# Kernel tuning notes

Measured on AMD Instinct MI355X. Metric: run time of the kernel, lower is better.

The kernel has to match this reference:

```python
import jax, jax.numpy as jnp
import numpy as np

DIM = 1024
NUM_HEADS = 16
NUM_KV_HEADS = 4
HEAD_DIM = DIM // NUM_HEADS  # 64
QK_GAIN = 1.5
ROPE_BASE = 10000.0


def _rms_norm(x, eps):
    # F.rms_norm with no weight: x / sqrt(mean(x^2) + eps)
    ms = jnp.mean(jnp.square(x), axis=-1, keepdims=True)
    return x * jax.lax.rsqrt(ms + eps)


def _rope_tables(seqlen, dim, dtype):
    inv_freq = 1.0 / (ROPE_BASE ** (jnp.arange(0, dim, 2, dtype=jnp.float32) / dim))
    freqs = jnp.outer(jnp.arange(seqlen, dtype=jnp.float32), inv_freq)  # [N, D/2]
    emb = jnp.concatenate([freqs, freqs], axis=-1)  # [N, D]
    return jnp.cos(emb).astype(dtype), jnp.sin(emb).astype(dtype)


def _apply_rope(x, cos, sin):
    # x: [B, N, H, D]; cos/sin: [N, D] broadcast over batch and heads
    half = x.shape[-1] // 2
    rot = jnp.concatenate([-x[..., half:], x[..., :half]], axis=-1)
    return x * cos[None, :, None, :] + rot * sin[None, :, None, :]


def setup_inputs() -> dict:
    key = jax.random.key(0)
    ks = jax.random.split(key, 5)
    B, N, C = 4, 2048, DIM
    s = 0.02
    return {
        "x": jax.random.normal(ks[0], (B, N, C), dtype=jnp.float32),
        "wq": jax.random.normal(ks[1], (C, C), dtype=jnp.float32) * s,
        "wk": jax.random.normal(ks[2], (C, NUM_KV_HEADS * HEAD_DIM), dtype=jnp.float32) * s,
        "wv": jax.random.normal(ks[3], (C, NUM_KV_HEADS * HEAD_DIM), dtype=jnp.float32) * s,
        "wo": jax.random.normal(ks[4], (C, C), dtype=jnp.float32) * s,
    }


def reference(x, wq, wk, wv, wo) -> jnp.ndarray:
    B, N, C = x.shape
    H, Hkv, D = NUM_HEADS, NUM_KV_HEADS, HEAD_DIM
    eps = jnp.finfo(x.dtype).eps

    q = (x @ wq).reshape(B, N, H, D)
    k = (x @ wk).reshape(B, N, Hkv, D)
    v = (x @ wv).reshape(B, N, Hkv, D)

    q = _rms_norm(q, eps)
    k = _rms_norm(k, eps)

    cos, sin = _rope_tables(N, D, q.dtype)
    q = _apply_rope(q, cos, sin) * QK_GAIN
    k = _apply_rope(k, cos, sin)

    # GQA head expansion (repeat_interleave along head dim)
    g = H // Hkv
    k = jnp.repeat(k, g, axis=2)  # [B, N, H, D]
    v = jnp.repeat(v, g, axis=2)

    # causal SDPA, scale = 1/sqrt(D)
    scores = jnp.einsum("bqhd,bkhd->bhqk", q, k) / jnp.sqrt(jnp.asarray(D, q.dtype))
    causal = jnp.tril(jnp.ones((N, N), dtype=bool))
    scores = jnp.where(causal[None, None], scores, jnp.finfo(scores.dtype).min)
    probs = jax.nn.softmax(scores, axis=-1)
    y = jnp.einsum("bhqk,bkhd->bqhd", probs, v).reshape(B, N, C)
    return y @ wo
```

## Files before the change

kernel.cpp:

```cpp
#include <hip/hip_runtime.h>

typedef __bf16 bf16;
typedef __bf16 bf16x8 __attribute__((ext_vector_type(8)));
typedef __bf16 bf16x4 __attribute__((ext_vector_type(4)));
typedef float f32x4 __attribute__((ext_vector_type(4)));

#define B_ 4
#define N_ 2048
#define C_ 1024
#define H_ 16
#define HKV_ 4
#define D_ 64

#define QSCALE 0.2705053201666806f
#define NEGINF (-1.0e30f)

__global__ __launch_bounds__(256) void prep_qkv(const float* __restrict__ wq,
                                                const float* __restrict__ wk,
                                                const float* __restrict__ wv,
                                                bf16* __restrict__ wT) {
  __shared__ __align__(16) bf16 lds[64 * 72];
  int bx = blockIdx.x;
  const float* w;
  int ncols, tk, tn, nbase;
  if (bx < 256) {
    w = wq; ncols = 1024; tk = bx >> 4; tn = bx & 15; nbase = 0;
  } else if (bx < 320) {
    int t = bx - 256;
    w = wk; ncols = 256; tk = t >> 2; tn = t & 3; nbase = 1024;
  } else {
    int t = bx - 320;
    w = wv; ncols = 256; tk = t >> 2; tn = t & 3; nbase = 1280;
  }
  int tid = threadIdx.x;
#pragma unroll
  for (int i = 0; i < 4; ++i) {
    int c = tid + i * 256;
    int kr = c >> 4, n4 = (c & 15) * 4;
    f32x4 v = *(const f32x4*)(w + (size_t)(tk * 64 + kr) * ncols + tn * 64 + n4);
    bf16x4 b;
#pragma unroll
    for (int j = 0; j < 4; ++j) b[j] = (bf16)v[j];
    *(bf16x4*)(lds + kr * 72 + n4) = b;
  }
  __syncthreads();
#pragma unroll
  for (int i = 0; i < 2; ++i) {
    int c = tid + i * 256;
    int n = c >> 3, koff = (c & 7) * 8;
    bf16x8 tv;
#pragma unroll
    for (int j = 0; j < 8; ++j) tv[j] = lds[(koff + j) * 72 + n];
    *(bf16x8*)(wT + (size_t)(nbase + tn * 64 + n) * 1024 + tk * 64 + koff) = tv;
  }
}

__global__ __launch_bounds__(256) void prep_wo(const float* __restrict__ w,
                                               bf16* __restrict__ wT) {
  __shared__ __align__(16) bf16 lds[64 * 72];
  int tk = blockIdx.x >> 4, tn = blockIdx.x & 15;
  int tid = threadIdx.x;
#pragma unroll
  for (int i = 0; i < 4; ++i) {
    int c = tid + i * 256;
    int kr = c >> 4, n4 = (c & 15) * 4;
    f32x4 v = *(const f32x4*)(w + (size_t)(tk * 64 + kr) * 1024 + tn * 64 + n4);
    bf16x4 b;
#pragma unroll
    for (int j = 0; j < 4; ++j) b[j] = (bf16)v[j];
    *(bf16x4*)(lds + kr * 72 + n4) = b;
  }
  __syncthreads();
#pragma unroll
  for (int i = 0; i < 2; ++i) {
    int c = tid + i * 256;
    int n = c >> 3, koff = (c & 7) * 8;
    bf16x8 tv;
#pragma unroll
    for (int j = 0; j < 8; ++j) tv[j] = lds[(koff + j) * 72 + n];
    *(bf16x8*)(wT + (size_t)(tn * 64 + n) * 1024 + tk * 64 + koff) = tv;
  }
}

__global__ __launch_bounds__(256) void gemm_qkv(const float* __restrict__ x,
                                                const bf16* __restrict__ wT,
                                                bf16* __restrict__ qb,
                                                bf16* __restrict__ kvb) {
  __shared__ __align__(16) bf16 As[128 * 72];
  __shared__ __align__(16) bf16 Bs[128 * 72];
  int by = blockIdx.y;
  int n0 = by * 128;
  bf16* Out;
  int ostride, ocol0;
  if (by < 8) {
    Out = qb; ostride = 1024; ocol0 = by * 128;
  } else if (by < 10) {
    Out = kvb; ostride = 512; ocol0 = (by - 8) * 128;
  } else {
    Out = kvb; ostride = 512; ocol0 = 256 + (by - 10) * 128;
  }
  int m0 = blockIdx.x * 128;
  int tid = threadIdx.x;
  int wave = tid >> 6, lane = tid & 63;
  int quad = lane >> 4, lr = lane & 15;
  int wr = (wave >> 1) * 64, wc = (wave & 1) * 64;
  int arow = tid >> 4, aoff = (tid & 15) * 4;
  int brow = tid >> 3, boff = (tid & 7) * 8;

  f32x4 acc[4][4];
  const f32x4 z = {0.f, 0.f, 0.f, 0.f};
#pragma unroll
  for (int i = 0; i < 4; ++i)
#pragma unroll
    for (int j = 0; j < 4; ++j) acc[i][j] = z;

  f32x4 sa[8];
  bf16x8 sb[4];
#pragma unroll
  for (int i = 0; i < 8; ++i)
    sa[i] = *(const f32x4*)(x + (size_t)(m0 + arow + i * 16) * 1024 + aoff);
#pragma unroll
  for (int i = 0; i < 4; ++i)
    sb[i] = *(const bf16x8*)(wT + (size_t)(n0 + brow + i * 32) * 1024 + boff);
#pragma unroll
  for (int i = 0; i < 8; ++i) {
    bf16x4 a16;
#pragma unroll
    for (int j = 0; j < 4; ++j) a16[j] = (bf16)sa[i][j];
    *(bf16x4*)(As + (arow + i * 16) * 72 + aoff) = a16;
  }
#pragma unroll
  for (int i = 0; i < 4; ++i) *(bf16x8*)(Bs + (brow + i * 32) * 72 + boff) = sb[i];
  asm volatile("s_waitcnt lgkmcnt(0)" ::: "memory");
  __builtin_amdgcn_s_barrier();
  __builtin_amdgcn_sched_barrier(0);

  for (int k0 = 0; k0 < 1024; k0 += 64) {
    bool pf = (k0 + 64 < 1024);
    if (pf) {
#pragma unroll
      for (int i = 0; i < 8; ++i)
        sa[i] = *(const f32x4*)(x + (size_t)(m0 + arow + i * 16) * 1024 + k0 + 64 + aoff);
#pragma unroll
      for (int i = 0; i < 4; ++i)
        sb[i] = *(const bf16x8*)(wT + (size_t)(n0 + brow + i * 32) * 1024 + k0 + 64 + boff);
    }
#pragma unroll
    for (int kx = 0; kx < 2; ++kx) {
      bf16x8 af[4], bfr[4];
#pragma unroll
      for (int t = 0; t < 4; ++t) {
        af[t] = *(const bf16x8*)(As + (wr + t * 16 + lr) * 72 + kx * 32 + quad * 8);
        bfr[t] = *(const bf16x8*)(Bs + (wc + t * 16 + lr) * 72 + kx * 32 + quad * 8);
      }
      __builtin_amdgcn_s_setprio(1);
#pragma unroll
      for (int rt = 0; rt < 4; ++rt)
#pragma unroll
        for (int ct = 0; ct < 4; ++ct)
          acc[rt][ct] = __builtin_amdgcn_mfma_f32_16x16x32_bf16(af[rt], bfr[ct],
                                                                acc[rt][ct], 0, 0, 0);
      __builtin_amdgcn_s_setprio(0);
    }
    __builtin_amdgcn_s_barrier();
    __builtin_amdgcn_sched_barrier(0);
    if (pf) {
#pragma unroll
      for (int i = 0; i < 8; ++i) {
        bf16x4 a16;
#pragma unroll
        for (int j = 0; j < 4; ++j) a16[j] = (bf16)sa[i][j];
        *(bf16x4*)(As + (arow + i * 16) * 72 + aoff) = a16;
      }
#pragma unroll
      for (int i = 0; i < 4; ++i) *(bf16x8*)(Bs + (brow + i * 32) * 72 + boff) = sb[i];
      asm volatile("s_waitcnt lgkmcnt(0)" ::: "memory");
    }
    __builtin_amdgcn_s_barrier();
    __builtin_amdgcn_sched_barrier(0);
  }
#pragma unroll
  for (int rt = 0; rt < 4; ++rt)
#pragma unroll
    for (int ct = 0; ct < 4; ++ct)
#pragma unroll
      for (int r = 0; r < 4; ++r) {
        int row = m0 + wr + rt * 16 + quad * 4 + r;
        int col = ocol0 + wc + ct * 16 + lr;
        Out[(size_t)row * ostride + col] = (bf16)acc[rt][ct][r];
      }
}

__global__ __launch_bounds__(256) void gemm_out(const bf16* __restrict__ A,
                                                const bf16* __restrict__ Bt,
                                                float* __restrict__ C) {
  __shared__ __align__(16) bf16 As[128 * 72];
  __shared__ __align__(16) bf16 Bs[128 * 72];
  int m0 = blockIdx.x * 128, n0 = blockIdx.y * 128;
  int tid = threadIdx.x;
  int wave = tid >> 6, lane = tid & 63;
  int quad = lane >> 4, lr = lane & 15;
  int wr = (wave >> 1) * 64, wc = (wave & 1) * 64;
  int brow = tid >> 3, boff = (tid & 7) * 8;

  f32x4 acc[4][4];
  const f32x4 z = {0.f, 0.f, 0.f, 0.f};
#pragma unroll
  for (int i = 0; i < 4; ++i)
#pragma unroll
    for (int j = 0; j < 4; ++j) acc[i][j] = z;

  bf16x8 sa[4], sb[4];
#pragma unroll
  for (int i = 0; i < 4; ++i) {
    sa[i] = *(const bf16x8*)(A + (size_t)(m0 + brow + i * 32) * 1024 + boff);
    sb[i] = *(const bf16x8*)(Bt + (size_t)(n0 + brow + i * 32) * 1024 + boff);
  }
#pragma unroll
  for (int i = 0; i < 4; ++i) {
    *(bf16x8*)(As + (brow + i * 32) * 72 + boff) = sa[i];
    *(bf16x8*)(Bs + (brow + i * 32) * 72 + boff) = sb[i];
  }
  asm volatile("s_waitcnt lgkmcnt(0)" ::: "memory");
  __builtin_amdgcn_s_barrier();
  __builtin_amdgcn_sched_barrier(0);

  for (int k0 = 0; k0 < 1024; k0 += 64) {
    bool pf = (k0 + 64 < 1024);
    if (pf) {
#pragma unroll
      for (int i = 0; i < 4; ++i) {
        sa[i] = *(const bf16x8*)(A + (size_t)(m0 + brow + i * 32) * 1024 + k0 + 64 + boff);
        sb[i] = *(const bf16x8*)(Bt + (size_t)(n0 + brow + i * 32) * 1024 + k0 + 64 + boff);
      }
    }
#pragma unroll
    for (int kx = 0; kx < 2; ++kx) {
      bf16x8 af[4], bfr[4];
#pragma unroll
      for (int t = 0; t < 4; ++t) {
        af[t] = *(const bf16x8*)(As + (wr + t * 16 + lr) * 72 + kx * 32 + quad * 8);
        bfr[t] = *(const bf16x8*)(Bs + (wc + t * 16 + lr) * 72 + kx * 32 + quad * 8);
      }
      __builtin_amdgcn_s_setprio(1);
#pragma unroll
      for (int rt = 0; rt < 4; ++rt)
#pragma unroll
        for (int ct = 0; ct < 4; ++ct)
          acc[rt][ct] = __builtin_amdgcn_mfma_f32_16x16x32_bf16(af[rt], bfr[ct],
                                                                acc[rt][ct], 0, 0, 0);
      __builtin_amdgcn_s_setprio(0);
    }
    __builtin_amdgcn_s_barrier();
    __builtin_amdgcn_sched_barrier(0);
    if (pf) {
#pragma unroll
      for (int i = 0; i < 4; ++i) {
        *(bf16x8*)(As + (brow + i * 32) * 72 + boff) = sa[i];
        *(bf16x8*)(Bs + (brow + i * 32) * 72 + boff) = sb[i];
      }
      asm volatile("s_waitcnt lgkmcnt(0)" ::: "memory");
    }
    __builtin_amdgcn_s_barrier();
    __builtin_amdgcn_sched_barrier(0);
  }
#pragma unroll
  for (int rt = 0; rt < 4; ++rt)
#pragma unroll
    for (int ct = 0; ct < 4; ++ct)
#pragma unroll
      for (int r = 0; r < 4; ++r) {
        int row = m0 + wr + rt * 16 + quad * 4 + r;
        int col = n0 + wc + ct * 16 + lr;
        C[(size_t)row * 1024 + col] = acc[rt][ct][r];
      }
}

__global__ __launch_bounds__(256) void transpose_v(const bf16* __restrict__ kv,
                                                   bf16* __restrict__ vt) {
  __shared__ __align__(16) bf16 lds[64 * 72];
  int nt = blockIdx.x;
  int bh = blockIdx.y;
  int b = bh >> 2, hkv = bh & 3;
  int tid = threadIdx.x;
#pragma unroll
  for (int i = 0; i < 2; ++i) {
    int c = tid + i * 256;
    int tok = c >> 3, off = (c & 7) * 8;
    *(bf16x8*)(lds + tok * 72 + off) =
        *(const bf16x8*)(kv + (size_t)(b * N_ + nt * 64 + tok) * 512 + 256 + hkv * 64 + off);
  }
  __syncthreads();
#pragma unroll
  for (int i = 0; i < 2; ++i) {
    int c = tid + i * 256;
    int d = c >> 3, toff = (c & 7) * 8;
    bf16x8 tv;
#pragma unroll
    for (int j = 0; j < 8; ++j) tv[j] = lds[(toff + j) * 72 + d];
    *(bf16x8*)(vt + ((size_t)bh * 64 + d) * N_ + nt * 64 + toff) = tv;
  }
}

__global__ __launch_bounds__(256) void norm_rope(bf16* __restrict__ q,
                                                 bf16* __restrict__ kv) {
  int tid = threadIdx.x;
  int g = (blockIdx.x << 5) + (tid >> 3);
  int e = tid & 7;
  int t = g / 20;
  int sub = g - t * 20;
  int n = t & (N_ - 1);
  bf16* ptr;
  float oscale;
  if (sub < 16) {
    ptr = q + (size_t)t * 1024 + sub * 64;
    oscale = QSCALE;
  } else {
    ptr = kv + (size_t)t * 512 + (sub - 16) * 64;
    oscale = 1.0f;
  }
  bf16x8 v = *(const bf16x8*)(ptr + e * 8);
  float xv[8];
  float ss = 0.f;
#pragma unroll
  for (int i = 0; i < 8; ++i) {
    xv[i] = (float)v[i];
    ss += xv[i] * xv[i];
  }
  ss += __shfl_xor(ss, 1);
  ss += __shfl_xor(ss, 2);
  ss += __shfl_xor(ss, 4);
  float rn = rsqrtf(ss * (1.0f / 64.0f) + 1.1920929e-07f);
  float base = (float)((e & 3) * 8);
  bf16x8 o;
#pragma unroll
  for (int i = 0; i < 8; ++i) {
    float xn = xv[i] * rn;
    float pr = __shfl_xor(xn, 4);
    float rot = (e < 4) ? -pr : pr;
    float ang = (float)n * exp2f(-0.41524101186092029f * (base + (float)i));
    float sv, cv;
    __sincosf(ang, &sv, &cv);
    o[i] = (bf16)((xn * cv + rot * sv) * oscale);
  }
  *(bf16x8*)(ptr + e * 8) = o;
}

__global__ __launch_bounds__(256) void attn(bf16* __restrict__ q,
                                            const bf16* __restrict__ kv,
                                            const bf16* __restrict__ vt) {
  __shared__ __align__(16) bf16 Ks[64 * 64];
  __shared__ __align__(16) bf16 Vs[64 * 64];
  __shared__ __align__(16) bf16 Ps[64 * 64];
  int bid = blockIdx.x;
  int orig = (bid & 7) * 128 + (bid >> 3);
  int grp = orig >> 6;
  int inner = orig & 63;
  int b = grp >> 2, hkv = grp & 3;
  int h = hkv * 4 + (inner & 3);
  int p = inner >> 2;
  int tid = threadIdx.x;
  int wave = tid >> 6, lane = tid & 63;
  int quad = lane >> 4, lr = lane & 15;
  int srow = tid >> 3, soff = (tid & 7) * 8;
  int su = ((tid & 7) ^ (srow & 7)) * 8;
  int e7 = lr & 7;
  const f32x4 z = {0.f, 0.f, 0.f, 0.f};

#pragma unroll 1
  for (int s = 0; s < 2; ++s) {
    int j = s ? (31 - p) : p;
    __syncthreads();
    int qrow0 = j * 64 + wave * 16;
    int nkt = j + 1;

    bf16x8 qf[2];
#pragma unroll
    for (int kx = 0; kx < 2; ++kx)
      qf[kx] = *(const bf16x8*)(
          q + ((size_t)(b * N_ + qrow0 + lr) * H_ + h) * D_ + kx * 32 + quad * 8);

    f32x4 acc[4];
    float l_i = 0.f;
#pragma unroll
    for (int dt = 0; dt < 4; ++dt) acc[dt] = z;

    const bf16* kp = kv + (size_t)(b * N_ + srow) * 512 + hkv * 64 + soff;
    const bf16* vp = vt + ((size_t)(b * HKV_ + hkv) * 64 + srow) * N_ + soff;

    bf16x8 sk0, sk1, sv0, sv1;
    sk0 = *(const bf16x8*)(kp);
    sk1 = *(const bf16x8*)(kp + 32 * 512);
    sv0 = *(const bf16x8*)(vp);
    sv1 = *(const bf16x8*)(vp + 32 * N_);
    *(bf16x8*)(Ks + srow * 64 + su) = sk0;
    *(bf16x8*)(Ks + (srow + 32) * 64 + su) = sk1;
    *(bf16x8*)(Vs + srow * 64 + su) = sv0;
    *(bf16x8*)(Vs + (srow + 32) * 64 + su) = sv1;
    asm volatile("s_waitcnt lgkmcnt(0)" ::: "memory");
    __builtin_amdgcn_s_barrier();
    __builtin_amdgcn_sched_barrier(0);

    for (int kt = 0; kt < nkt; ++kt) {
      bool pf = (kt + 1 < nkt);
      if (pf) {
        kp += 64 * 512;
        vp += 64;
        sk0 = *(const bf16x8*)(kp);
        sk1 = *(const bf16x8*)(kp + 32 * 512);
        sv0 = *(const bf16x8*)(vp);
        sv1 = *(const bf16x8*)(vp + 32 * N_);
      }

      f32x4 st[4];
#pragma unroll
      for (int ct = 0; ct < 4; ++ct) st[ct] = z;
#pragma unroll
      for (int kx = 0; kx < 2; ++kx) {
        bf16x8 kf[4];
#pragma unroll
        for (int ct = 0; ct < 4; ++ct)
          kf[ct] = *(const bf16x8*)(Ks + (ct * 16 + lr) * 64 + (((kx * 4 + quad) ^ e7) * 8));
        __builtin_amdgcn_s_setprio(1);
#pragma unroll
        for (int ct = 0; ct < 4; ++ct)
          st[ct] = __builtin_amdgcn_mfma_f32_16x16x32_bf16(kf[ct], qf[kx], st[ct], 0, 0, 0);
        __builtin_amdgcn_s_setprio(0);
      }
      if (kt == j) {
        int qrow = qrow0 + lr;
#pragma unroll
        for (int ct = 0; ct < 4; ++ct)
#pragma unroll
          for (int r = 0; r < 4; ++r) {
            int key = kt * 64 + ct * 16 + quad * 4 + r;
            if (key > qrow) st[ct][r] = NEGINF;
          }
      }
      float rs = 0.f;
#pragma unroll
      for (int ct = 0; ct < 4; ++ct)
#pragma unroll
        for (int r = 0; r < 4; ++r) {
          float pv = exp2f(st[ct][r]);
          st[ct][r] = pv;
          rs += pv;
        }
      rs += __shfl_xor(rs, 16);
      rs += __shfl_xor(rs, 32);
      l_i += rs;
#pragma unroll
      for (int ct = 0; ct < 4; ++ct) {
        bf16x4 pk;
#pragma unroll
        for (int r = 0; r < 4; ++r) pk[r] = (bf16)st[ct][r];
        int pu = (((ct * 2) + (quad >> 1)) ^ e7) * 8 + (quad & 1) * 4;
        *(bf16x4*)(Ps + (wave * 16 + lr) * 64 + pu) = pk;
      }
      asm volatile("s_waitcnt lgkmcnt(0)" ::: "memory");
#pragma unroll
      for (int kx = 0; kx < 2; ++kx) {
        bf16x8 vf[4], pfr;
#pragma unroll
        for (int dt = 0; dt < 4; ++dt)
          vf[dt] = *(const bf16x8*)(Vs + (dt * 16 + lr) * 64 + (((kx * 4 + quad) ^ e7) * 8));
        pfr = *(const bf16x8*)(Ps + (wave * 16 + lr) * 64 + (((kx * 4 + quad) ^ e7) * 8));
        __builtin_amdgcn_s_setprio(1);
#pragma unroll
        for (int dt = 0; dt < 4; ++dt)
          acc[dt] = __builtin_amdgcn_mfma_f32_16x16x32_bf16(vf[dt], pfr, acc[dt], 0, 0, 0);
        __builtin_amdgcn_s_setprio(0);
      }

      __builtin_amdgcn_s_barrier();
      __builtin_amdgcn_sched_barrier(0);
      if (pf) {
        *(bf16x8*)(Ks + srow * 64 + su) = sk0;
        *(bf16x8*)(Ks + (srow + 32) * 64 + su) = sk1;
        *(bf16x8*)(Vs + srow * 64 + su) = sv0;
        *(bf16x8*)(Vs + (srow + 32) * 64 + su) = sv1;
        asm volatile("s_waitcnt lgkmcnt(0)" ::: "memory");
      }
      __builtin_amdgcn_s_barrier();
      __builtin_amdgcn_sched_barrier(0);
    }

    float inv = 1.0f / l_i;
    int qrow = qrow0 + lr;
#pragma unroll
    for (int dt = 0; dt < 4; ++dt) {
      bf16x4 ov;
#pragma unroll
      for (int r = 0; r < 4; ++r) ov[r] = (bf16)(acc[dt][r] * inv);
      *(bf16x4*)(q + ((size_t)(b * N_ + qrow) * H_ + h) * D_ + dt * 16 + quad * 4) = ov;
    }
  }
}

extern "C" void kernel_launch(void* const* d_in, const int* in_sizes, int n_in,
                              void* d_out, int out_size, void* d_ws, size_t ws_size,
                              hipStream_t stream) {
  const float* x = (const float*)d_in[0];
  const float* wq = (const float*)d_in[1];
  const float* wk = (const float*)d_in[2];
  const float* wv = (const float*)d_in[3];
  const float* wo = (const float*)d_in[4];
  float* out = (float*)d_out;
  char* ws = (char*)d_ws;
  bf16* q = (bf16*)(ws);
  bf16* kv = (bf16*)(ws + 16777216);
  bf16* vt = (bf16*)(ws + 25165824);
  bf16* wqkvT = (bf16*)(ws + 25165824);
  bf16* woT = (bf16*)(ws + 25165824);

  prep_qkv<<<dim3(384), 256, 0, stream>>>(wq, wk, wv, wqkvT);
  gemm_qkv<<<dim3(64, 12), 256, 0, stream>>>(x, wqkvT, q, kv);
  norm_rope<<<dim3(5120), 256, 0, stream>>>(q, kv);
  transpose_v<<<dim3(32, 16), 256, 0, stream>>>(kv, vt);
  attn<<<dim3(1024), 256, 0, stream>>>(q, kv, vt);
  prep_wo<<<dim3(256), 256, 0, stream>>>(wo, woT);
  gemm_out<<<dim3(64, 8), 256, 0, stream>>>(q, woT, out);
}
```

Baseline: 247.1 us.

## Double-buffer K/V shared-memory tiles in attention to drop a barrier per step

Shared-memory K and V tiles become two ping-pong buffers. The next tile is written into the alternate buffer after the current tile's compute, and the following tile's global loads are issued one iteration earlier. This removes one of the two block barriers per key tile and gives global loads a full iteration to land. In exchange it doubles K/V LDS use (about 40KB total), which may reduce occupancy, and register pressure rises slightly.

```diff
diff --git a/kernel.cpp b/kernel.cpp
--- a/kernel.cpp
+++ b/kernel.cpp
@@ -349,8 +349,8 @@
 __global__ __launch_bounds__(256) void attn(bf16* __restrict__ q,
                                             const bf16* __restrict__ kv,
                                             const bf16* __restrict__ vt) {
-  __shared__ __align__(16) bf16 Ks[64 * 64];
-  __shared__ __align__(16) bf16 Vs[64 * 64];
+  __shared__ __align__(16) bf16 Ks[2][64 * 64];
+  __shared__ __align__(16) bf16 Vs[2][64 * 64];
   __shared__ __align__(16) bf16 Ps[64 * 64];
   int bid = blockIdx.x;
   int orig = (bid & 7) * 128 + (bid >> 3);
@@ -393,25 +393,26 @@
     sk1 = *(const bf16x8*)(kp + 32 * 512);
     sv0 = *(const bf16x8*)(vp);
     sv1 = *(const bf16x8*)(vp + 32 * N_);
-    *(bf16x8*)(Ks + srow * 64 + su) = sk0;
-    *(bf16x8*)(Ks + (srow + 32) * 64 + su) = sk1;
-    *(bf16x8*)(Vs + srow * 64 + su) = sv0;
-    *(bf16x8*)(Vs + (srow + 32) * 64 + su) = sv1;
+    *(bf16x8*)(Ks[0] + srow * 64 + su) = sk0;
+    *(bf16x8*)(Ks[0] + (srow + 32) * 64 + su) = sk1;
+    *(bf16x8*)(Vs[0] + srow * 64 + su) = sv0;
+    *(bf16x8*)(Vs[0] + (srow + 32) * 64 + su) = sv1;
+    if (nkt > 1) {
+      kp += 64 * 512;
+      vp += 64;
+      sk0 = *(const bf16x8*)(kp);
+      sk1 = *(const bf16x8*)(kp + 32 * 512);
+      sv0 = *(const bf16x8*)(vp);
+      sv1 = *(const bf16x8*)(vp + 32 * N_);
+    }
     asm volatile("s_waitcnt lgkmcnt(0)" ::: "memory");
     __builtin_amdgcn_s_barrier();
     __builtin_amdgcn_sched_barrier(0);
 
+    int cur = 0;
     for (int kt = 0; kt < nkt; ++kt) {
-      bool pf = (kt + 1 < nkt);
-      if (pf) {
-        kp += 64 * 512;
-        vp += 64;
-        sk0 = *(const bf16x8*)(kp);
-        sk1 = *(const bf16x8*)(kp + 32 * 512);
-        sv0 = *(const bf16x8*)(vp);
-        sv1 = *(const bf16x8*)(vp + 32 * N_);
-      }
-
+      const bf16* Kc = Ks[cur];
+      const bf16* Vc = Vs[cur];
       f32x4 st[4];
 #pragma unroll
       for (int ct = 0; ct < 4; ++ct) st[ct] = z;
@@ -420,7 +421,7 @@
         bf16x8 kf[4];
 #pragma unroll
         for (int ct = 0; ct < 4; ++ct)
-          kf[ct] = *(const bf16x8*)(Ks + (ct * 16 + lr) * 64 + (((kx * 4 + quad) ^ e7) * 8));
+          kf[ct] = *(const bf16x8*)(Kc + (ct * 16 + lr) * 64 + (((kx * 4 + quad) ^ e7) * 8));
         __builtin_amdgcn_s_setprio(1);
 #pragma unroll
         for (int ct = 0; ct < 4; ++ct)
@@ -463,7 +464,7 @@
         bf16x8 vf[4], pfr;
 #pragma unroll
         for (int dt = 0; dt < 4; ++dt)
-          vf[dt] = *(const bf16x8*)(Vs + (dt * 16 + lr) * 64 + (((kx * 4 + quad) ^ e7) * 8));
+          vf[dt] = *(const bf16x8*)(Vc + (dt * 16 + lr) * 64 + (((kx * 4 + quad) ^ e7) * 8));
         pfr = *(const bf16x8*)(Ps + (wave * 16 + lr) * 64 + (((kx * 4 + quad) ^ e7) * 8));
         __builtin_amdgcn_s_setprio(1);
 #pragma unroll
@@ -472,17 +473,27 @@
         __builtin_amdgcn_s_setprio(0);
       }
 
+      bool pf = (kt + 1 < nkt);
+      if (pf) {
+        bf16* Kn = Ks[cur ^ 1];
+        bf16* Vn = Vs[cur ^ 1];
+        *(bf16x8*)(Kn + srow * 64 + su) = sk0;
+        *(bf16x8*)(Kn + (srow + 32) * 64 + su) = sk1;
+        *(bf16x8*)(Vn + srow * 64 + su) = sv0;
+        *(bf16x8*)(Vn + (srow + 32) * 64 + su) = sv1;
+        if (kt + 2 < nkt) {
+          kp += 64 * 512;
+          vp += 64;
+          sk0 = *(const bf16x8*)(kp);
+          sk1 = *(const bf16x8*)(kp + 32 * 512);
+          sv0 = *(const bf16x8*)(vp);
+          sv1 = *(const bf16x8*)(vp + 32 * N_);
+        }
+        asm volatile("s_waitcnt lgkmcnt(0)" ::: "memory");
+      }
       __builtin_amdgcn_s_barrier();
       __builtin_amdgcn_sched_barrier(0);
-      if (pf) {
-        *(bf16x8*)(Ks + srow * 64 + su) = sk0;
-        *(bf16x8*)(Ks + (srow + 32) * 64 + su) = sk1;
-        *(bf16x8*)(Vs + srow * 64 + su) = sv0;
-        *(bf16x8*)(Vs + (srow + 32) * 64 + su) = sv1;
-        asm volatile("s_waitcnt lgkmcnt(0)" ::: "memory");
-      }
-      __builtin_amdgcn_s_barrier();
-      __builtin_amdgcn_sched_barrier(0);
+      cur ^= 1;
     }
 
     float inv = 1.0f / l_i;
```

New measurement: 255.3 us. +3.3%, slower.
